# Kernel optimization log

Measured on AMD Instinct MI355X. Metric: run time of the kernel, lower is better.

## Reference

```python
import jax, jax.numpy as jnp
import numpy as np

B, L, D, H = 4, 1024, 1024, 16
DH = D // H
NEG = -1e9


def setup_inputs() -> dict:
    key = jax.random.key(0)
    ks = jax.random.split(key, 8)
    sequence = jax.random.normal(ks[0], (B, L, D), dtype=jnp.float32)
    # additive padding mask: all tokens valid -> zeros
    padding_mask = jnp.zeros((B, 1, 1, L), dtype=jnp.float32)
    # additive causal dependency mask: -1e9 above the diagonal
    causal = jnp.triu(jnp.full((L, L), NEG, dtype=jnp.float32), k=1)
    dependency_mask = causal[None, None, :, :]
    scale = 1.0 / np.sqrt(D)
    Wq = jax.random.normal(ks[1], (D, D), dtype=jnp.float32) * scale
    Wk = jax.random.normal(ks[2], (D, D), dtype=jnp.float32) * scale
    Wv = jax.random.normal(ks[3], (D, D), dtype=jnp.float32) * scale
    bq = jnp.zeros((D,), dtype=jnp.float32)
    bk = jnp.zeros((D,), dtype=jnp.float32)
    bv = jnp.zeros((D,), dtype=jnp.float32)
    return {"sequence": sequence, "padding_mask": padding_mask,
            "dependency_mask": dependency_mask,
            "Wq": Wq, "bq": bq, "Wk": Wk, "bk": bk, "Wv": Wv, "bv": bv}


def reference(sequence, padding_mask, dependency_mask, Wq, bq, Wk, bk, Wv, bv):
    b, l, d = sequence.shape
    h, dh = H, d // H
    # Q/K/V linear projections (torch Linear: x @ W^T + b)
    q = (sequence @ Wq.T + bq).reshape(b, l, h, dh)
    k = (sequence @ Wk.T + bk).reshape(b, l, h, dh)
    v = (sequence @ Wv.T + bv).reshape(b, l, h, dh)
    # scaled dot-product scores: [B, H, L, L]
    scores = jnp.einsum('blhd,bmhd->bhlm', q, k) / jnp.sqrt(jnp.float32(dh))
    scores = scores + padding_mask + dependency_mask
    attn = jax.nn.softmax(scores, axis=-1)
    # dropout is identity in eval mode (training=False)
    out = jnp.einsum('bhlm,bmhd->blhd', attn, v)
    return out.reshape(b, l, d)
```

## Files before the change

### kernel.cpp

```cpp
#include <hip/hip_runtime.h>
#include <hip/hip_bf16.h>


#define LL 1024

typedef __attribute__((ext_vector_type(8))) short short8;
typedef __attribute__((ext_vector_type(4))) float floatx4;

__device__ __forceinline__ float bf2f(unsigned short u) {
    return __uint_as_float(((unsigned int)u) << 16);
}
__device__ __forceinline__ unsigned short f2bf(float f) {
    unsigned int x = __float_as_uint(f);
    unsigned int r = x + 0x7fffu + ((x >> 16) & 1u);
    return (unsigned short)(r >> 16);
}

#if __has_builtin(__builtin_amdgcn_global_load_lds)
#define HAVE_GLL 1
typedef __attribute__((address_space(1))) unsigned int as1_u32;
typedef __attribute__((address_space(3))) unsigned int as3_u32;
__device__ __forceinline__ void gll16(const void* g, void* l) {
    __builtin_amdgcn_global_load_lds((const as1_u32*)g, (as3_u32*)l, 16, 0, 0);
}
#endif

#if __has_builtin(__builtin_amdgcn_exp2f)
#define EXP2F(x) __builtin_amdgcn_exp2f(x)
#else
#define EXP2F(x) exp2f(x)
#endif

__global__ __launch_bounds__(256) void conv_in(
    const float* __restrict__ seq, const float* __restrict__ wq,
    const float* __restrict__ wk,  const float* __restrict__ wv,
    const float* __restrict__ bq,  const float* __restrict__ bk,
    const float* __restrict__ bv,  const float* __restrict__ pm,
    unsigned short* __restrict__ ws)
{
    unsigned int t = blockIdx.x * 256u + threadIdx.x;
    if (t >= 918400u) return;
    unsigned int e = t * 8u;
    const float* src; unsigned int idx; unsigned short* dst; float scale = 1.0f;
    if (e < 4194304u)      { src = seq; idx = e;            dst = ws + 12582912u; }
    else if (e < 5242880u) { src = wq;  idx = e - 4194304u; dst = ws + 16777216u; }
    else if (e < 6291456u) { src = wk;  idx = e - 5242880u; dst = ws + 17825792u; }
    else if (e < 7340032u) { src = wv;  idx = e - 6291456u; dst = ws + 18874368u; }
    else if (e < 7341056u) { src = bq;  idx = e - 7340032u; dst = ws + 20971520u; }
    else if (e < 7342080u) { src = bk;  idx = e - 7341056u; dst = ws + 20972544u; }
    else if (e < 7343104u) { src = bv;  idx = e - 7342080u; dst = ws + 20973568u; }
    else { src = pm; idx = e - 7343104u; dst = ws + 20974592u; scale = 1.4426950f; }
    float4 a = *(const float4*)(src + idx);
    float4 c = *(const float4*)(src + idx + 4);
    uint4 st;
    st.x = (unsigned)f2bf(a.x * scale) | ((unsigned)f2bf(a.y * scale) << 16);
    st.y = (unsigned)f2bf(a.z * scale) | ((unsigned)f2bf(a.w * scale) << 16);
    st.z = (unsigned)f2bf(c.x * scale) | ((unsigned)f2bf(c.y * scale) << 16);
    st.w = (unsigned)f2bf(c.z * scale) | ((unsigned)f2bf(c.w * scale) << 16);
    *(uint4*)(dst + idx) = st;
}

__global__ __launch_bounds__(512, 2) void qkv_proj(
    const unsigned short* __restrict__ X,
    const unsigned short* __restrict__ Wcat,
    const unsigned short* __restrict__ bcat,
    unsigned short* __restrict__ dst_base)
{
    __shared__ __align__(16) unsigned short Abuf[3][16384];
    __shared__ __align__(16) unsigned short Bbuf[2][12288];

    const int tid  = threadIdx.x;
    const int lane = tid & 63;
    const int wave = tid >> 6;
    const int quad = lane >> 4, r16 = lane & 15;
    const int wr = wave >> 2, wc = wave & 3;
    const int m0 = blockIdx.x * 256;
    const int n0 = blockIdx.y * 192;

    const int r3   = lane >> 3;
    const int stc  = ((lane & 7) ^ r3) << 3;
    const int seg0a = wave * 4;
    const int seg0b = wave * 3;

    const unsigned short* Asrc = X    + (size_t)(m0 + seg0a * 8 + r3) * 1024 + stc;
    const unsigned short* Bsrc = Wcat + (size_t)(n0 + seg0b * 8 + r3) * 1024 + stc;

    floatx4 acc[8][3];
#pragma unroll
    for (int i = 0; i < 8; ++i)
#pragma unroll
        for (int j = 0; j < 3; ++j)
#pragma unroll
            for (int r = 0; r < 4; ++r) acc[i][j][r] = 0.f;

#ifdef HAVE_GLL
#pragma unroll
    for (int c = 0; c < 4; ++c) gll16(Asrc + (size_t)c * 8192, &Abuf[0][(seg0a + c) * 512]);
#pragma unroll
    for (int c = 0; c < 3; ++c) gll16(Bsrc + (size_t)c * 8192, &Bbuf[0][(seg0b + c) * 512]);
#pragma unroll
    for (int c = 0; c < 4; ++c) gll16(Asrc + (size_t)c * 8192 + 64, &Abuf[1][(seg0a + c) * 512]);
    asm volatile("s_waitcnt vmcnt(4)" ::: "memory");
    __builtin_amdgcn_s_barrier();
#endif

    int sA = 0;
    for (int t = 0; t < 16; ++t) {
        const unsigned short* Ac = &Abuf[sA][0];
        const unsigned short* Bc = &Bbuf[t & 1][0];
        const int aoff = (wr * 128 + r16) * 64;
        const int boff = (wc * 48 + r16) * 64;
        const int c0 = ((0 + quad) ^ (r16 & 7)) << 3;
        const int c1 = ((4 + quad) ^ (r16 & 7)) << 3;
        short8 a[4], b[3];

#ifndef HAVE_GLL
        __syncthreads();
#pragma unroll
        for (int c = 0; c < 4; ++c)
            *(uint4*)&Abuf[0][(seg0a + c) * 512 + lane * 8] =
                *(const uint4*)(Asrc + (size_t)c * 8192 + (t << 6));
#pragma unroll
        for (int c = 0; c < 3; ++c)
            *(uint4*)&Bbuf[0][(seg0b + c) * 512 + lane * 8] =
                *(const uint4*)(Bsrc + (size_t)c * 8192 + (t << 6));
        __syncthreads();
        Ac = &Abuf[0][0]; Bc = &Bbuf[0][0];
#endif

#pragma unroll
        for (int i = 0; i < 4; ++i) a[i] = *(const short8*)&Ac[aoff + i * 1024 + c0];
#pragma unroll
        for (int j = 0; j < 3; ++j) b[j] = *(const short8*)&Bc[boff + j * 1024 + c0];
#ifdef HAVE_GLL
        if (t < 15) {
            const int sBw = (t + 1) & 1;
            const size_t ko = (size_t)((t + 1) << 6);
#pragma unroll
            for (int c = 0; c < 3; ++c)
                gll16(Bsrc + (size_t)c * 8192 + ko, &Bbuf[sBw][(seg0b + c) * 512]);
        }
        __builtin_amdgcn_s_barrier();
        asm volatile("s_waitcnt lgkmcnt(0)" ::: "memory");
#endif
        __builtin_amdgcn_s_setprio(1);
#pragma unroll
        for (int i = 0; i < 4; ++i)
#pragma unroll
            for (int j = 0; j < 3; ++j)
                acc[i][j] = __builtin_amdgcn_mfma_f32_16x16x32_bf16(a[i], b[j], acc[i][j], 0, 0, 0);
        __builtin_amdgcn_s_setprio(0);
#ifdef HAVE_GLL
        __builtin_amdgcn_s_barrier();
#endif

#pragma unroll
        for (int i = 0; i < 4; ++i) a[i] = *(const short8*)&Ac[aoff + (4 + i) * 1024 + c0];
#ifdef HAVE_GLL
        if (t < 14) {
            const int sAw = (sA == 0) ? 2 : (sA - 1);
            const size_t ko = (size_t)((t + 2) << 6);
#pragma unroll
            for (int c = 0; c < 4; ++c)
                gll16(Asrc + (size_t)c * 8192 + ko, &Abuf[sAw][(seg0a + c) * 512]);
        }
        __builtin_amdgcn_s_barrier();
        asm volatile("s_waitcnt lgkmcnt(0)" ::: "memory");
#endif
        __builtin_amdgcn_s_setprio(1);
#pragma unroll
        for (int i = 0; i < 4; ++i)
#pragma unroll
            for (int j = 0; j < 3; ++j)
                acc[4 + i][j] = __builtin_amdgcn_mfma_f32_16x16x32_bf16(a[i], b[j], acc[4 + i][j], 0, 0, 0);
        __builtin_amdgcn_s_setprio(0);
#ifdef HAVE_GLL
        __builtin_amdgcn_s_barrier();
#endif

#pragma unroll
        for (int i = 0; i < 4; ++i) a[i] = *(const short8*)&Ac[aoff + i * 1024 + c1];
#pragma unroll
        for (int j = 0; j < 3; ++j) b[j] = *(const short8*)&Bc[boff + j * 1024 + c1];
#ifdef HAVE_GLL
        __builtin_amdgcn_s_barrier();
        asm volatile("s_waitcnt lgkmcnt(0)" ::: "memory");
#endif
        __builtin_amdgcn_s_setprio(1);
#pragma unroll
        for (int i = 0; i < 4; ++i)
#pragma unroll
            for (int j = 0; j < 3; ++j)
                acc[i][j] = __builtin_amdgcn_mfma_f32_16x16x32_bf16(a[i], b[j], acc[i][j], 0, 0, 0);
        __builtin_amdgcn_s_setprio(0);
#ifdef HAVE_GLL
        __builtin_amdgcn_s_barrier();
#endif

#pragma unroll
        for (int i = 0; i < 4; ++i) a[i] = *(const short8*)&Ac[aoff + (4 + i) * 1024 + c1];
#ifdef HAVE_GLL
        __builtin_amdgcn_s_barrier();
        asm volatile("s_waitcnt lgkmcnt(0)" ::: "memory");
#endif
        __builtin_amdgcn_s_setprio(1);
#pragma unroll
        for (int i = 0; i < 4; ++i)
#pragma unroll
            for (int j = 0; j < 3; ++j)
                acc[4 + i][j] = __builtin_amdgcn_mfma_f32_16x16x32_bf16(a[i], b[j], acc[4 + i][j], 0, 0, 0);
        __builtin_amdgcn_s_setprio(0);
#ifdef HAVE_GLL
        if (t < 14) {
            asm volatile("s_waitcnt vmcnt(4)" ::: "memory");
        } else if (t == 14) {
            asm volatile("s_waitcnt vmcnt(0)" ::: "memory");
        }
        __builtin_amdgcn_s_barrier();
#endif
        sA = (sA == 2) ? 0 : (sA + 1);
    }

#pragma unroll
    for (int j = 0; j < 3; ++j) {
        int n = n0 + wc * 48 + j * 16 + r16;
        int z = n >> 10;
        int nn = n & 1023;
        float bvf = bf2f(bcat[n]);
        float sc = (z == 0) ? 0.18033688f : 1.0f;
        int h = nn >> 6, d = nn & 63;
        unsigned short* dst = dst_base + (size_t)z * (4096u * 1024u);
#pragma unroll
        for (int i = 0; i < 8; ++i) {
            int m_base = m0 + wr * 128 + i * 16 + quad * 4;
            int bb = m_base >> 10, l0 = m_base & 1023;
            if (z == 2) {
                ushort4 st;
                st.x = f2bf(acc[i][j][0] + bvf); st.y = f2bf(acc[i][j][1] + bvf);
                st.z = f2bf(acc[i][j][2] + bvf); st.w = f2bf(acc[i][j][3] + bvf);
                *(ushort4*)&dst[(((size_t)(bb * 16 + h)) * 64 + d) * 1024 + l0] = st;
            } else {
#pragma unroll
                for (int r = 0; r < 4; ++r)
                    dst[(((size_t)(bb * 16 + h)) * 1024 + (l0 + r)) * 64 + d] =
                        f2bf((acc[i][j][r] + bvf) * sc);
            }
        }
    }
}

__global__ __launch_bounds__(256) void attn(
    const unsigned short* __restrict__ Qw,
    const unsigned short* __restrict__ Kw,
    const unsigned short* __restrict__ Vt_g,
    const unsigned short* __restrict__ pmask,
    float* __restrict__ out)
{
    __shared__ __align__(16) unsigned short KsF[8192];
    __shared__ __align__(16) unsigned short VsF[8192];
    __shared__ __align__(16) unsigned short PsF[2][4][2048];

    const int tid  = threadIdx.x;
    const int lane = tid & 63;
    const int wave = tid >> 6;
    const int quad = lane >> 4, r16 = lane & 15;

    const int bid  = blockIdx.x;
    const int half = bid >> 8, idx = bid & 255;
    const int bh   = idx & 63;
    const int qb   = idx >> 6;
    const int qi   = half ? (7 - qb) : qb;
    const int b    = bh >> 4, h = bh & 15;
    const int q0   = qi << 7;

    const size_t base = (size_t)bh * (1024 * 64);
    const unsigned short* Qg = Qw + base;
    const unsigned short* Kg = Kw + base;
    const unsigned short* Vg = Vt_g + base;

    const int kst_r3  = lane >> 3;
    const int kst_col = ((lane & 7) ^ kst_r3) << 3;
    const int vst_r   = lane >> 4;

    short8 aq[2][2];
#pragma unroll
    for (int f = 0; f < 2; ++f) {
        int qrow = q0 + f * 64 + wave * 16 + r16;
        aq[f][0] = *(const short8*)(Qg + (size_t)qrow * 64 + quad * 8);
        aq[f][1] = *(const short8*)(Qg + (size_t)qrow * 64 + 32 + quad * 8);
    }

    short8 ones;
#pragma unroll
    for (int i = 0; i < 8; ++i) ones[i] = (short)0x3f80;

    floatx4 ol[2];
    floatx4 o[2][4];
#pragma unroll
    for (int f = 0; f < 2; ++f)
#pragma unroll
        for (int r = 0; r < 4; ++r) ol[f][r] = 0.f;
#pragma unroll
    for (int f = 0; f < 2; ++f)
#pragma unroll
        for (int j = 0; j < 4; ++j)
#pragma unroll
            for (int r = 0; r < 4; ++r) o[f][j][r] = 0.f;

    for (int kt = 0; kt <= qi; ++kt) {
        float pm2[8];
#pragma unroll
        for (int j = 0; j < 8; ++j)
            pm2[j] = bf2f(pmask[b * LL + kt * 128 + j * 16 + r16]) - 12.0f;

        __syncthreads();
#ifdef HAVE_GLL
#pragma unroll
        for (int c2 = 0; c2 < 4; ++c2) {
            int seg = wave * 4 + c2;
            int krow = seg * 8 + kst_r3;
            gll16(Kg + (size_t)(kt * 128 + krow) * 64 + kst_col, &KsF[seg * 512]);
            int vrow = seg * 4 + vst_r;
            int vcol = (((lane & 15) ^ (vrow & 7))) << 3;
            gll16(Vg + (size_t)vrow * 1024 + kt * 128 + vcol, &VsF[seg * 512]);
        }
#else
#pragma unroll
        for (int c2 = 0; c2 < 4; ++c2) {
            int seg = wave * 4 + c2;
            int krow = seg * 8 + kst_r3;
            *(uint4*)&KsF[seg * 512 + lane * 8] =
                *(const uint4*)(Kg + (size_t)(kt * 128 + krow) * 64 + kst_col);
            int vrow = seg * 4 + vst_r;
            int vcol = (((lane & 15) ^ (vrow & 7))) << 3;
            *(uint4*)&VsF[seg * 512 + lane * 8] =
                *(const uint4*)(Vg + (size_t)vrow * 1024 + kt * 128 + vcol);
        }
#endif
        __syncthreads();

#pragma unroll
        for (int f = 0; f < 2; ++f) {
            floatx4 s[8];
#pragma unroll
            for (int j = 0; j < 8; ++j)
#pragma unroll
                for (int r = 0; r < 4; ++r) s[j][r] = 0.f;
#pragma unroll
            for (int j = 0; j < 8; ++j) {
                short8 bk0 = *(const short8*)&KsF[(j * 16 + r16) * 64 + (((0 * 4 + quad) ^ (r16 & 7)) << 3)];
                s[j] = __builtin_amdgcn_mfma_f32_16x16x32_bf16(aq[f][0], bk0, s[j], 0, 0, 0);
                short8 bk1 = *(const short8*)&KsF[(j * 16 + r16) * 64 + (((1 * 4 + quad) ^ (r16 & 7)) << 3)];
                s[j] = __builtin_amdgcn_mfma_f32_16x16x32_bf16(aq[f][1], bk1, s[j], 0, 0, 0);
            }

            if (kt == qi) {
                const int my_q = q0 + f * 64 + wave * 16 + quad * 4;
#pragma unroll
                for (int j = 0; j < 8; ++j) {
                    int key = kt * 128 + j * 16 + r16;
#pragma unroll
                    for (int r = 0; r < 4; ++r)
                        if (key > my_q + r) s[j][r] -= 1.0e9f;
                }
            }

#pragma unroll
            for (int j = 0; j < 8; ++j) {
                int key = j * 16 + r16;
                int ab = ((key >> 5) << 9) + (((key >> 3) & 3) << 7) + (key & 7) + (quad << 5);
#pragma unroll
                for (int r = 0; r < 4; ++r) {
                    float p = EXP2F(s[j][r] + pm2[j]);
                    PsF[f][wave][ab + (r << 3)] = (unsigned short)(__float_as_uint(p) >> 16);
                }
            }
            asm volatile("s_waitcnt lgkmcnt(0)" ::: "memory");

#pragma unroll
            for (int kk4 = 0; kk4 < 4; ++kk4) {
                short8 ap = *(const short8*)&PsF[f][wave][kk4 * 512 + lane * 8];
                ol[f] = __builtin_amdgcn_mfma_f32_16x16x32_bf16(ap, ones, ol[f], 0, 0, 0);
#pragma unroll
                for (int j2 = 0; j2 < 4; ++j2) {
                    short8 bv = *(const short8*)&VsF[(j2 * 16 + r16) * 128 + (((kk4 * 4 + quad) ^ (r16 & 7)) << 3)];
                    o[f][j2] = __builtin_amdgcn_mfma_f32_16x16x32_bf16(ap, bv, o[f][j2], 0, 0, 0);
                }
            }
        }
    }

#pragma unroll
    for (int f = 0; f < 2; ++f) {
        float linv[4];
#pragma unroll
        for (int r = 0; r < 4; ++r)
            linv[r] = 1.0f / fmaxf(ol[f][r], 1.0e-30f);
        const int my_q = q0 + f * 64 + wave * 16 + quad * 4;
#pragma unroll
        for (int j2 = 0; j2 < 4; ++j2) {
            int d = j2 * 16 + r16;
#pragma unroll
            for (int r = 0; r < 4; ++r) {
                size_t oidx = ((size_t)(b * 1024 + my_q + r)) * 1024 + h * 64 + d;
                out[oidx] = o[f][j2][r] * linv[r];
            }
        }
    }
}

__global__ __launch_bounds__(256) void fill_sentinel_f(float* __restrict__ out,
                                                       float v, unsigned int n)
{
    unsigned int t = blockIdx.x * 256u + threadIdx.x;
    if (t < n) out[t] = v;
}

extern "C" void kernel_launch(void* const* d_in, const int* in_sizes, int n_in,
                              void* d_out, int out_size, void* d_ws, size_t ws_size,
                              hipStream_t stream) {
    bool sizes_ok = (n_in == 9) && in_sizes[0] == 4194304 && in_sizes[1] == 4096 &&
                    in_sizes[2] == 1048576 && in_sizes[3] == 1048576 && in_sizes[4] == 1024 &&
                    in_sizes[5] == 1048576 && in_sizes[6] == 1024 && in_sizes[7] == 1048576 &&
                    in_sizes[8] == 1024 && out_size == 4194304;
    if (!sizes_ok) {
        fill_sentinel_f<<<16384, 256, 0, stream>>>((float*)d_out, 100.0f, 4194304u);
        return;
    }
    if (ws_size < 50331652u) {
        fill_sentinel_f<<<16384, 256, 0, stream>>>((float*)d_out, 200.0f, 4194304u);
        return;
    }

    unsigned short* ws = (unsigned short*)d_ws;

    conv_in<<<3588, 256, 0, stream>>>(
        (const float*)d_in[0], (const float*)d_in[3], (const float*)d_in[5],
        (const float*)d_in[7], (const float*)d_in[4], (const float*)d_in[6],
        (const float*)d_in[8], (const float*)d_in[1], ws);

    const unsigned short* cseq  = ws + 12582912u;
    const unsigned short* cwcat = ws + 16777216u;
    const unsigned short* cbcat = ws + 20971520u;
    const unsigned short* cpm   = ws + 20974592u;

    dim3 g1(16, 16);
    qkv_proj<<<g1, 512, 0, stream>>>(cseq, cwcat, cbcat, ws);

    attn<<<512, 256, 0, stream>>>(ws, ws + 4194304u, ws + 8388608u, cpm, (float*)d_out);
}
```

Measured before the change: 150.1 us.

## Double-buffer K tiles and prefetch next K during attention compute

Restructures the attention loop so the next K tile is loaded into a second LDS buffer while the current tile is processed. V loads are issued early and waited on with partial vmcnt counts before the PV stage. The padding mask is staged once into LDS instead of being read from global memory every iteration, the P buffer is shrunk to a single per-wave slot, and MFMA sections are wrapped in s_setprio. This trades simpler barrier logic for hand-counted vmcnt waits. It may read one K tile past the valid range on the last iteration.

```diff
diff --git a/kernel.cpp b/kernel.cpp
--- a/kernel.cpp
+++ b/kernel.cpp
@@ -256,9 +256,10 @@
     const unsigned short* __restrict__ pmask,
     float* __restrict__ out)
 {
-    __shared__ __align__(16) unsigned short KsF[8192];
-    __shared__ __align__(16) unsigned short VsF[8192];
-    __shared__ __align__(16) unsigned short PsF[2][4][2048];
+    __shared__ __align__(16) unsigned short Ks[2][8192];
+    __shared__ __align__(16) unsigned short Vs[8192];
+    __shared__ __align__(16) unsigned short Ps[4][2048];
+    __shared__ __align__(16) unsigned short PMs[1024];
 
     const int tid  = threadIdx.x;
     const int lane = tid & 63;
@@ -307,37 +308,65 @@
 #pragma unroll
             for (int r = 0; r < 4; ++r) o[f][j][r] = 0.f;
 
+#ifdef HAVE_GLL
+    gll16(pmask + (size_t)b * LL + lane * 8,       &PMs[0]);
+    gll16(pmask + (size_t)b * LL + 512 + lane * 8, &PMs[512]);
+    asm volatile("" ::: "memory");
+#pragma unroll
+    for (int c2 = 0; c2 < 4; ++c2) {
+        int seg = wave * 4 + c2;
+        int krow = seg * 8 + kst_r3;
+        gll16(Kg + (size_t)krow * 64 + kst_col, &Ks[0][seg * 512]);
+    }
+    asm volatile("" ::: "memory");
+#else
+    if (tid < 128) {
+        *(uint4*)&PMs[tid * 8] = *(const uint4*)(pmask + (size_t)b * LL + tid * 8);
+    }
+    __syncthreads();
+#endif
+
     for (int kt = 0; kt <= qi; ++kt) {
-        float pm2[8];
-#pragma unroll
-        for (int j = 0; j < 8; ++j)
-            pm2[j] = bf2f(pmask[b * LL + kt * 128 + j * 16 + r16]) - 12.0f;
-
-        __syncthreads();
-#ifdef HAVE_GLL
+        const int cur = kt & 1;
+        const int nxt = cur ^ 1;
+
+#ifdef HAVE_GLL
+#pragma unroll
+        for (int c2 = 0; c2 < 4; ++c2) {
+            int seg = wave * 4 + c2;
+            int vrow = seg * 4 + vst_r;
+            int vcol = (((lane & 15) ^ (vrow & 7))) << 3;
+            gll16(Vg + (size_t)vrow * 1024 + kt * 128 + vcol, &Vs[seg * 512]);
+        }
+        asm volatile("" ::: "memory");
 #pragma unroll
         for (int c2 = 0; c2 < 4; ++c2) {
             int seg = wave * 4 + c2;
             int krow = seg * 8 + kst_r3;
-            gll16(Kg + (size_t)(kt * 128 + krow) * 64 + kst_col, &KsF[seg * 512]);
-            int vrow = seg * 4 + vst_r;
-            int vcol = (((lane & 15) ^ (vrow & 7))) << 3;
-            gll16(Vg + (size_t)vrow * 1024 + kt * 128 + vcol, &VsF[seg * 512]);
-        }
+            gll16(Kg + (size_t)((kt + 1) * 128 + krow) * 64 + kst_col, &Ks[nxt][seg * 512]);
+        }
+        asm volatile("s_waitcnt vmcnt(8)" ::: "memory");
+        __builtin_amdgcn_s_barrier();
 #else
+        __syncthreads();
 #pragma unroll
         for (int c2 = 0; c2 < 4; ++c2) {
             int seg = wave * 4 + c2;
             int krow = seg * 8 + kst_r3;
-            *(uint4*)&KsF[seg * 512 + lane * 8] =
+            *(uint4*)&Ks[0][seg * 512 + lane * 8] =
                 *(const uint4*)(Kg + (size_t)(kt * 128 + krow) * 64 + kst_col);
             int vrow = seg * 4 + vst_r;
             int vcol = (((lane & 15) ^ (vrow & 7))) << 3;
-            *(uint4*)&VsF[seg * 512 + lane * 8] =
+            *(uint4*)&Vs[seg * 512 + lane * 8] =
                 *(const uint4*)(Vg + (size_t)vrow * 1024 + kt * 128 + vcol);
         }
-#endif
         __syncthreads();
+#endif
+
+        float pm2[8];
+#pragma unroll
+        for (int j = 0; j < 8; ++j)
+            pm2[j] = bf2f(PMs[kt * 128 + j * 16 + r16]) - 12.0f;
 
 #pragma unroll
         for (int f = 0; f < 2; ++f) {
@@ -346,13 +375,20 @@
             for (int j = 0; j < 8; ++j)
 #pragma unroll
                 for (int r = 0; r < 4; ++r) s[j][r] = 0.f;
+            __builtin_amdgcn_s_setprio(1);
 #pragma unroll
             for (int j = 0; j < 8; ++j) {
-                short8 bk0 = *(const short8*)&KsF[(j * 16 + r16) * 64 + (((0 * 4 + quad) ^ (r16 & 7)) << 3)];
+#ifdef HAVE_GLL
+                const unsigned short* Kc = &Ks[cur][0];
+#else
+                const unsigned short* Kc = &Ks[0][0];
+#endif
+                short8 bk0 = *(const short8*)&Kc[(j * 16 + r16) * 64 + (((0 * 4 + quad) ^ (r16 & 7)) << 3)];
                 s[j] = __builtin_amdgcn_mfma_f32_16x16x32_bf16(aq[f][0], bk0, s[j], 0, 0, 0);
-                short8 bk1 = *(const short8*)&KsF[(j * 16 + r16) * 64 + (((1 * 4 + quad) ^ (r16 & 7)) << 3)];
+                short8 bk1 = *(const short8*)&Kc[(j * 16 + r16) * 64 + (((1 * 4 + quad) ^ (r16 & 7)) << 3)];
                 s[j] = __builtin_amdgcn_mfma_f32_16x16x32_bf16(aq[f][1], bk1, s[j], 0, 0, 0);
             }
+            __builtin_amdgcn_s_setprio(0);
 
             if (kt == qi) {
                 const int my_q = q0 + f * 64 + wave * 16 + quad * 4;
@@ -372,23 +408,40 @@
 #pragma unroll
                 for (int r = 0; r < 4; ++r) {
                     float p = EXP2F(s[j][r] + pm2[j]);
-                    PsF[f][wave][ab + (r << 3)] = (unsigned short)(__float_as_uint(p) >> 16);
+                    Ps[wave][ab + (r << 3)] = (unsigned short)(__float_as_uint(p) >> 16);
                 }
             }
             asm volatile("s_waitcnt lgkmcnt(0)" ::: "memory");
 
+#ifdef HAVE_GLL
+            if (f == 0) {
+                asm volatile("s_waitcnt vmcnt(4)" ::: "memory");
+                __builtin_amdgcn_s_barrier();
+            }
+#endif
+
+            __builtin_amdgcn_s_setprio(1);
 #pragma unroll
             for (int kk4 = 0; kk4 < 4; ++kk4) {
-                short8 ap = *(const short8*)&PsF[f][wave][kk4 * 512 + lane * 8];
+                short8 ap = *(const short8*)&Ps[wave][kk4 * 512 + lane * 8];
                 ol[f] = __builtin_amdgcn_mfma_f32_16x16x32_bf16(ap, ones, ol[f], 0, 0, 0);
 #pragma unroll
                 for (int j2 = 0; j2 < 4; ++j2) {
-                    short8 bv = *(const short8*)&VsF[(j2 * 16 + r16) * 128 + (((kk4 * 4 + quad) ^ (r16 & 7)) << 3)];
+                    short8 bv = *(const short8*)&Vs[(j2 * 16 + r16) * 128 + (((kk4 * 4 + quad) ^ (r16 & 7)) << 3)];
                     o[f][j2] = __builtin_amdgcn_mfma_f32_16x16x32_bf16(ap, bv, o[f][j2], 0, 0, 0);
                 }
             }
-        }
-    }
+            __builtin_amdgcn_s_setprio(0);
+        }
+
+#ifdef HAVE_GLL
+        __builtin_amdgcn_s_barrier();
+#endif
+    }
+
+#ifdef HAVE_GLL
+    asm volatile("s_waitcnt vmcnt(0)" ::: "memory");
+#endif
 
 #pragma unroll
     for (int f = 0; f < 2; ++f) {
```

After: 151.7 us. No clear change (+1.0%).
